# Optimization experiments

Measured on AMD Instinct MI355X. Metric: run time of the kernel, lower is better.

## Reference

```python
import jax, jax.numpy as jnp
import numpy as np

B, L, D, HD = 4, 4096, 2048, 128

def setup_inputs() -> dict:
    key = jax.random.key(0)
    ks = jax.random.split(key, 9)
    s = 0.02  # keep logits in a sane range
    return {
        "x": jax.random.normal(ks[0], (B, L, D), jnp.float32),
        "Wq": jax.random.normal(ks[1], (D, HD), jnp.float32) * s,
        "bq": jax.random.normal(ks[2], (HD,), jnp.float32) * s,
        "Wk": jax.random.normal(ks[3], (D, HD), jnp.float32) * s,
        "bk": jax.random.normal(ks[4], (HD,), jnp.float32) * s,
        "Wv": jax.random.normal(ks[5], (D, HD), jnp.float32) * s,
        "bv": jax.random.normal(ks[6], (HD,), jnp.float32) * s,
        "Wo": jax.random.normal(ks[7], (HD, D), jnp.float32) * s,
        "bo": jax.random.normal(ks[8], (D,), jnp.float32) * s,
    }

def reference(x, Wq, bq, Wk, bk, Wv, bv, Wo, bo):
    # x: (B, L, D)
    q = x @ Wq + bq                      # (B, L, HD)
    k = x @ Wk + bk
    v = x @ Wv + bv
    hd = q.shape[-1]
    scores = jnp.einsum('bqd,bkd->bqk', q, k) / jnp.sqrt(jnp.float32(hd))
    Lq = x.shape[1]
    causal = jnp.tril(jnp.ones((Lq, Lq), dtype=bool))  # (L, L)
    scores = jnp.where(causal, scores, -jnp.inf)
    weights = jax.nn.softmax(scores, axis=-1)          # (B, L, L)
    out = jnp.einsum('bqk,bkd->bqd', weights, v)       # (B, L, HD)
    return out @ Wo + bo                               # (B, L, D)
```

## Files before the change

kernel.cpp:

```cpp
#include <hip/hip_runtime.h>

#define B_  4
#define L_  4096
#define D_  2048
#define HD_ 128
#define M_  (B_*L_)

typedef __attribute__((ext_vector_type(8))) short short8;
typedef __attribute__((ext_vector_type(4))) float f32x4;
typedef __attribute__((ext_vector_type(16))) float f32x16;
typedef __attribute__((ext_vector_type(4))) unsigned short u16x4;
typedef __attribute__((ext_vector_type(4))) unsigned int u32x4;
typedef unsigned short u16;

__device__ __forceinline__ u16 f2bf(float f){
  union { float f; unsigned u; } v; v.f = f;
  unsigned r = v.u + 0x7FFFu + ((v.u >> 16) & 1u);
  return (u16)(r >> 16);
}

__device__ __forceinline__ unsigned cvtpk_bf16(float a, float b){
  unsigned r;
  asm volatile("v_cvt_pk_bf16_f32 %0, %1, %2" : "=v"(r) : "v"(a), "v"(b));
  return r;
}

__global__ __launch_bounds__(256) void prepw_kernel(
    const float* __restrict__ Wq, const float* __restrict__ Wk,
    const float* __restrict__ Wv, const float* __restrict__ Wo,
    u16* __restrict__ Wf_qkv, u16* __restrict__ Wf_o)
{
  __shared__ float T[64][68];
  const int tid = threadIdx.x;
  int tb = blockIdx.x;
  int mat = tb >> 6, tt = tb & 63;
  const float* src; int Cw, rt, ct;
  if (mat < 3) {
    src = (mat==0) ? Wq : (mat==1) ? Wk : Wv;
    Cw = HD_; rt = tt >> 1; ct = tt & 1;
  } else {
    src = Wo;
    Cw = D_; rt = tt >> 5; ct = tt & 31;
  }
  int r0 = rt*64, c0 = ct*64;
  #pragma unroll
  for (int i=0;i<4;i++){
    int fid = i*256 + tid;
    int row = fid >> 4, c4 = (fid & 15) * 4;
    float4 v = *reinterpret_cast<const float4*>(src + (size_t)(r0+row)*Cw + c0 + c4);
    *reinterpret_cast<float4*>(&T[row][c4]) = v;
  }
  __syncthreads();
  #pragma unroll
  for (int i=0;i<2;i++){
    int sid = i*256 + tid;
    int crow = sid >> 3, k8 = (sid & 7) * 8;
    short8 o;
    #pragma unroll
    for (int j=0;j<8;j++) o[j] = (short)f2bf(T[k8+j][crow]);
    int K = r0 + k8;
    if (mat < 3) {
      int C = mat*128 + c0 + crow;
      size_t off = ((size_t)(K>>4)*12 + (C>>5))*512
                 + ((((K>>3)&1))*32 + (C&31))*8;
      *reinterpret_cast<short8*>(Wf_qkv + off) = o;
    } else {
      int C = c0 + crow;
      size_t off = ((size_t)(K>>5)*128 + (C>>4))*512
                 + ((((K>>3)&3))*16 + (C&15))*8;
      *reinterpret_cast<short8*>(Wf_o + off) = o;
    }
  }
}

__global__ __launch_bounds__(256) void prepx_kernel(
    const float* __restrict__ x, u16* __restrict__ xbf)
{
  int cid  = blockIdx.x*4 + (threadIdx.x >> 6);
  int lane = threadIdx.x & 63;
  int l31 = lane & 31, hi = lane >> 5;
  int rs = cid >> 7, t = cid & 127;
  const float* src = x + (size_t)(rs*32 + l31)*D_ + t*16 + hi*8;
  float4 f0 = *reinterpret_cast<const float4*>(src);
  float4 f1 = *reinterpret_cast<const float4*>(src + 4);
  union { u32x4 u; short8 s8; } o;
  o.u[0] = cvtpk_bf16(f0.x, f0.y);
  o.u[1] = cvtpk_bf16(f0.z, f0.w);
  o.u[2] = cvtpk_bf16(f1.x, f1.y);
  o.u[3] = cvtpk_bf16(f1.z, f1.w);
  *reinterpret_cast<short8*>(xbf + (size_t)cid*512 + lane*8) = o.s8;
}

__global__ __launch_bounds__(256, 2) void qkv_kernel(
    const u16* __restrict__ xbf, const u16* __restrict__ Wf,
    const float* __restrict__ bq, const float* __restrict__ bk,
    const float* __restrict__ bv,
    u16* __restrict__ Q, u16* __restrict__ Kf, u16* __restrict__ Vf)
{
  const int rb = blockIdx.x;
  const int tid = threadIdx.x;
  const int lane = tid & 63, wc = tid >> 6;
  const int l31 = lane & 31, hi = lane >> 5;

  const u16* aP0 = xbf + ((size_t)(rb*2    )*128)*512 + lane*8;
  const u16* aP1 = xbf + ((size_t)(rb*2 + 1)*128)*512 + lane*8;
  const u16* bP  = Wf  + (size_t)(wc*3)*512 + lane*8;

  f32x16 acc[2][3];
  #pragma unroll
  for (int m=0;m<2;m++)
    #pragma unroll
    for (int nb=0;nb<3;nb++)
      #pragma unroll
      for (int i=0;i<16;i++) acc[m][nb][i] = 0.f;

  short8 a0 = *reinterpret_cast<const short8*>(aP0);
  short8 a1 = *reinterpret_cast<const short8*>(aP1);
  short8 b0 = *reinterpret_cast<const short8*>(bP);
  short8 b1 = *reinterpret_cast<const short8*>(bP + 512);
  short8 b2 = *reinterpret_cast<const short8*>(bP + 1024);

  for (int t = 0; t < 127; ++t) {
    short8 na0 = *reinterpret_cast<const short8*>(aP0 + (size_t)(t+1)*512);
    short8 na1 = *reinterpret_cast<const short8*>(aP1 + (size_t)(t+1)*512);
    const u16* nb_ = bP + (size_t)(t+1)*12*512;
    short8 nb0 = *reinterpret_cast<const short8*>(nb_);
    short8 nb1 = *reinterpret_cast<const short8*>(nb_ + 512);
    short8 nb2 = *reinterpret_cast<const short8*>(nb_ + 1024);
    __builtin_amdgcn_s_setprio(1);
    acc[0][0] = __builtin_amdgcn_mfma_f32_32x32x16_bf16(a0, b0, acc[0][0], 0, 0, 0);
    acc[0][1] = __builtin_amdgcn_mfma_f32_32x32x16_bf16(a0, b1, acc[0][1], 0, 0, 0);
    acc[0][2] = __builtin_amdgcn_mfma_f32_32x32x16_bf16(a0, b2, acc[0][2], 0, 0, 0);
    acc[1][0] = __builtin_amdgcn_mfma_f32_32x32x16_bf16(a1, b0, acc[1][0], 0, 0, 0);
    acc[1][1] = __builtin_amdgcn_mfma_f32_32x32x16_bf16(a1, b1, acc[1][1], 0, 0, 0);
    acc[1][2] = __builtin_amdgcn_mfma_f32_32x32x16_bf16(a1, b2, acc[1][2], 0, 0, 0);
    __builtin_amdgcn_s_setprio(0);
    a0 = na0; a1 = na1; b0 = nb0; b1 = nb1; b2 = nb2;
  }
  __builtin_amdgcn_s_setprio(1);
  acc[0][0] = __builtin_amdgcn_mfma_f32_32x32x16_bf16(a0, b0, acc[0][0], 0, 0, 0);
  acc[0][1] = __builtin_amdgcn_mfma_f32_32x32x16_bf16(a0, b1, acc[0][1], 0, 0, 0);
  acc[0][2] = __builtin_amdgcn_mfma_f32_32x32x16_bf16(a0, b2, acc[0][2], 0, 0, 0);
  acc[1][0] = __builtin_amdgcn_mfma_f32_32x32x16_bf16(a1, b0, acc[1][0], 0, 0, 0);
  acc[1][1] = __builtin_amdgcn_mfma_f32_32x32x16_bf16(a1, b1, acc[1][1], 0, 0, 0);
  acc[1][2] = __builtin_amdgcn_mfma_f32_32x32x16_bf16(a1, b2, acc[1][2], 0, 0, 0);
  __builtin_amdgcn_s_setprio(0);

  const float qscale = 0.08838834764831845f;
  const int bb = rb >> 6, kt = rb & 63;
  const size_t kvBase = ((size_t)bb*64 + kt)*16;
  #pragma unroll
  for (int nb=0; nb<3; nb++){
    const int colbase = wc*96 + nb*32;
    const int j = colbase >> 7;
    const int col = colbase + l31;
    const int c = col & 127;
    const float bi = (j==0) ? bq[c] : (j==1) ? bk[c] : bv[c];
    #pragma unroll
    for (int m=0;m<2;m++){
      if (j == 0) {
        #pragma unroll
        for (int r=0;r<16;r++){
          int row = rb*64 + m*32 + 4*hi + (r&3) + 8*(r>>2);
          Q[(size_t)row*HD_ + c] = f2bf((acc[m][nb][r] + bi) * qscale);
        }
      } else if (j == 1) {
        int ksd = c >> 4, hid = (c >> 3) & 1, jd = c & 7;
        #pragma unroll
        for (int r=0;r<16;r++){
          int l31k = 8*(r>>2) + 4*hi + (r&3);
          Kf[(kvBase + m*8 + ksd)*512 + (hid*32 + l31k)*8 + jd]
              = f2bf(acc[m][nb][r] + bi);
        }
      } else {
        int nbv = c >> 5;
        #pragma unroll
        for (int g=0; g<4; g++){
          int ksv = m*2 + (g>>1), hiv = g&1, j0 = 4*hi;
          u16x4 v4;
          #pragma unroll
          for (int q=0;q<4;q++) v4[q] = f2bf(acc[m][nb][4*g+q] + bi);
          *reinterpret_cast<u16x4*>(
              Vf + (kvBase + ksv*4 + nbv)*512 + (hiv*32 + l31)*8 + j0) = v4;
        }
      }
    }
  }
}

__global__ __launch_bounds__(256, 2) void attn_kernel(
    const u16* __restrict__ Qg, const u16* __restrict__ Kfg,
    const u16* __restrict__ Vfg, u16* __restrict__ AOf)
{
  const int blk = blockIdx.x;
  const int xcd = blk & 7;
  const int sub = blk >> 3;
  const int b   = xcd >> 1;
  const int strip = 127 - (2*sub + (xcd & 1));
  const int q0  = strip * 32;
  const int KT  = (strip >> 1) + 1;

  const int tid = threadIdx.x, lane = tid & 63, w = tid >> 6;
  const int l31 = lane & 31;
  const int hi  = lane >> 5;

  const u16* Qb  = Qg  + (size_t)b * L_ * HD_;
  const u16* Kfb = Kfg + (size_t)b * 64 * 8192 + lane*8;
  const u16* Vfb = Vfg + (size_t)b * 64 * 8192 + lane*8;

  __shared__ __attribute__((aligned(16))) float Ol[4][32][132];
  __shared__ float Ml[4][32], Ll[4][32];

  short8 qf[8];
  #pragma unroll
  for (int ks=0; ks<8; ks++)
    qf[ks] = *reinterpret_cast<const short8*>(
        &Qb[(size_t)(q0 + l31)*HD_ + ks*16 + hi*8]);

  f32x16 O[4];
  #pragma unroll
  for (int nb=0; nb<4; nb++)
    #pragma unroll
    for (int i=0;i<16;i++) O[nb][i] = 0.f;
  float m_ = -__builtin_inff();
  float l_ = 0.f;

  for (int kt = w; kt < KT; kt += 4) {
    const u16* Kt = Kfb + (size_t)kt*8192;
    f32x16 s[2];
    #pragma unroll
    for (int n=0;n<2;n++)
      #pragma unroll
      for (int i=0;i<16;i++) s[n][i] = 0.f;
    __builtin_amdgcn_s_setprio(1);
    #pragma unroll
    for (int ks=0;ks<8;ks++)
      #pragma unroll
      for (int n=0;n<2;n++){
        short8 ka = *reinterpret_cast<const short8*>(Kt + (n*8 + ks)*512);
        s[n] = __builtin_amdgcn_mfma_f32_32x32x16_bf16(ka, qf[ks], s[n], 0, 0, 0);
      }
    __builtin_amdgcn_s_setprio(0);

    if (kt == KT-1) {
      #pragma unroll
      for (int n=0;n<2;n++)
        #pragma unroll
        for (int reg=0;reg<16;reg++){
          int key = kt*64 + n*32 + (reg&3) + 8*(reg>>2) + 4*hi;
          if (key > q0 + l31) s[n][reg] = -__builtin_inff();
        }
    }

    float pmax = s[0][0];
    #pragma unroll
    for (int n=0;n<2;n++)
      #pragma unroll
      for (int reg=0;reg<16;reg++) pmax = fmaxf(pmax, s[n][reg]);
    pmax = fmaxf(pmax, __shfl_xor(pmax, 32, 64));

    if (!__all(pmax <= m_ + 8.f)) {
      float mnew = fmaxf(m_, pmax);
      float alpha = __expf(m_ - mnew);
      m_ = mnew;
      l_ *= alpha;
      #pragma unroll
      for (int nb=0; nb<4; nb++)
        #pragma unroll
        for (int i=0;i<16;i++) O[nb][i] *= alpha;
    }

    float rsum = 0.f;
    #pragma unroll
    for (int n=0;n<2;n++)
      #pragma unroll
      for (int reg=0;reg<16;reg++){
        float p = __expf(s[n][reg] - m_);
        s[n][reg] = p;
        rsum += p;
      }
    rsum += __shfl_xor(rsum, 32, 64);
    l_ += rsum;

    unsigned c[2][8], ox[2][8];
    #pragma unroll
    for (int n=0;n<2;n++)
      #pragma unroll
      for (int i=0;i<8;i++)
        c[n][i] = cvtpk_bf16(s[n][2*i], s[n][2*i+1]);
    #pragma unroll
    for (int n=0;n<2;n++)
      #pragma unroll
      for (int i=0;i<8;i++)
        ox[n][i] = (unsigned)__shfl_xor((int)c[n][i], 32, 64);

    short8 pb[4];
    #pragma unroll
    for (int n=0;n<2;n++)
      #pragma unroll
      for (int sB=0;sB<2;sB++){
        union { u32x4 u; short8 s8; } t;
        t.u[0] = hi ? ox[n][4*sB+2] : c[n][4*sB+0];
        t.u[1] = hi ? ox[n][4*sB+3] : c[n][4*sB+1];
        t.u[2] = hi ? c[n][4*sB+2]  : ox[n][4*sB+0];
        t.u[3] = hi ? c[n][4*sB+3]  : ox[n][4*sB+1];
        pb[2*n+sB] = t.s8;
      }

    const u16* Vt2 = Vfb + (size_t)kt*8192;
    __builtin_amdgcn_s_setprio(1);
    #pragma unroll
    for (int ks=0; ks<4; ks++){
      #pragma unroll
      for (int nb=0; nb<4; nb++){
        short8 av = *reinterpret_cast<const short8*>(Vt2 + (ks*4 + nb)*512);
        O[nb] = __builtin_amdgcn_mfma_f32_32x32x16_bf16(av, pb[ks], O[nb], 0, 0, 0);
      }
    }
    __builtin_amdgcn_s_setprio(0);
  }

  if (hi == 0) { Ml[w][l31] = m_; Ll[w][l31] = l_; }
  #pragma unroll
  for (int nb=0; nb<4; nb++)
    #pragma unroll
    for (int g=0; g<4; g++){
      f32x4 v;
      v[0]=O[nb][4*g+0]; v[1]=O[nb][4*g+1]; v[2]=O[nb][4*g+2]; v[3]=O[nb][4*g+3];
      *reinterpret_cast<f32x4*>(&Ol[w][l31][nb*32 + g*8 + hi*4]) = v;
    }
  __syncthreads();

  {
    int q  = tid >> 3;
    int dc = (tid & 7) * 16;
    float mw[4], lw[4];
    float M = -__builtin_inff();
    #pragma unroll
    for (int w2=0; w2<4; w2++){ mw[w2]=Ml[w2][q]; lw[w2]=Ll[w2][q]; M = fmaxf(M, mw[w2]); }
    float den = 0.f, cw[4];
    #pragma unroll
    for (int w2=0; w2<4; w2++){ float e = __expf(mw[w2]-M); cw[w2]=e; den += lw[w2]*e; }
    float inv = 1.0f/den;
    float o[16];
    #pragma unroll
    for (int j=0;j<16;j++) o[j] = 0.f;
    #pragma unroll
    for (int w2=0; w2<4; w2++){
      #pragma unroll
      for (int g=0; g<4; g++){
        f32x4 p = *reinterpret_cast<const f32x4*>(&Ol[w2][q][dc + g*4]);
        #pragma unroll
        for (int j=0;j<4;j++) o[g*4+j] += cw[w2]*p[j];
      }
    }
    short8 st0, st1;
    #pragma unroll
    for (int j=0;j<8;j++){ st0[j] = (short)f2bf(o[j]*inv); st1[j] = (short)f2bf(o[8+j]*inv); }
    size_t rowg = (size_t)b*L_ + q0 + q;
    size_t rb2g = rowg >> 5;
    int qq = (int)(rowg & 31);
    int mA = qq >> 4, l15A = qq & 15;
    int ks0 = dc >> 5,      lh0 = (dc >> 3) & 3;
    int ks1 = (dc+8) >> 5,  lh1 = ((dc+8) >> 3) & 3;
    *reinterpret_cast<short8*>(AOf + ((rb2g*4 + ks0)*2 + mA)*512 + (lh0*16 + l15A)*8) = st0;
    *reinterpret_cast<short8*>(AOf + ((rb2g*4 + ks1)*2 + mA)*512 + (lh1*16 + l15A)*8) = st1;
  }
}

__global__ __launch_bounds__(256) void proj_kernel(
    const u16* __restrict__ AOf, const u16* __restrict__ Wf_o,
    const float* __restrict__ bo, float* __restrict__ out)
{
  const int nb  = blockIdx.x;
  const int rbk = blockIdx.y;
  const int tid = threadIdx.x, lane = tid & 63, w = tid >> 6;
  const int l15 = lane & 15, lhi = lane >> 4;

  const u16* faBase = AOf  + (size_t)rbk*8*512 + lane*8;
  const u16* fbBase = Wf_o + lane*8;

  f32x4 acc[2][4];
  f32x4 zero4 = {0.f,0.f,0.f,0.f};
  #pragma unroll
  for (int m=0;m<2;m++)
    #pragma unroll
    for (int n=0;n<4;n++) acc[m][n] = zero4;

  #pragma unroll
  for (int ks=0; ks<4; ks++){
    short8 fa[2], fb[4];
    #pragma unroll
    for (int m=0;m<2;m++)
      fa[m] = *reinterpret_cast<const short8*>(faBase + (ks*2 + m)*512);
    #pragma unroll
    for (int n=0;n<4;n++)
      fb[n] = *reinterpret_cast<const short8*>(
          fbBase + (size_t)(ks*128 + nb*16 + w*4 + n)*512);
    #pragma unroll
    for (int m=0;m<2;m++)
      #pragma unroll
      for (int n=0;n<4;n++)
        acc[m][n] = __builtin_amdgcn_mfma_f32_16x16x32_bf16(fa[m], fb[n], acc[m][n], 0, 0, 0);
  }

  #pragma unroll
  for (int n=0;n<4;n++){
    int col = nb*256 + w*64 + n*16 + l15;
    float bi = bo[col];
    #pragma unroll
    for (int m=0;m<2;m++){
      int row = rbk*32 + m*16 + (lhi<<2);
      #pragma unroll
      for (int r=0;r<4;r++)
        out[(size_t)(row+r)*D_ + col] = acc[m][n][r] + bi;
    }
  }
}

extern "C" void kernel_launch(void* const* d_in, const int* in_sizes, int n_in,
                              void* d_out, int out_size, void* d_ws, size_t ws_size,
                              hipStream_t stream) {
  const float* x  = (const float*)d_in[0];
  const float* Wq = (const float*)d_in[1];
  const float* bq = (const float*)d_in[2];
  const float* Wk = (const float*)d_in[3];
  const float* bk = (const float*)d_in[4];
  const float* Wv = (const float*)d_in[5];
  const float* bv = (const float*)d_in[6];
  const float* Wo = (const float*)d_in[7];
  const float* bo = (const float*)d_in[8];
  float* out = (float*)d_out;

  u16* ws      = (u16*)d_ws;
  u16* Wf_qkv  = ws;
  u16* Wf_o    = Wf_qkv + 3*HD_*D_;
  u16* Q       = Wf_o   + (size_t)D_*HD_;
  u16* Kf      = Q + (size_t)M_*HD_;
  u16* Vf      = Kf + (size_t)M_*HD_;
  u16* AOf     = Vf + (size_t)M_*HD_;
  u16* xbf     = AOf + (size_t)M_*HD_;

  prepw_kernel<<<256, 256, 0, stream>>>(Wq, Wk, Wv, Wo, Wf_qkv, Wf_o);
  prepx_kernel<<<16384, 256, 0, stream>>>(x, xbf);
  qkv_kernel<<<256, 256, 0, stream>>>(xbf, Wf_qkv, bq, bk, bv, Q, Kf, Vf);
  attn_kernel<<<512, 256, 0, stream>>>(Q, Kf, Vf, AOf);
  proj_kernel<<<dim3(8, 512), 256, 0, stream>>>(AOf, Wf_o, bo, out);
}
```

Baseline: 195.8 us.

## Halve QKV row tile per block and deepen register prefetch pipeline

The QKV projection kernel now handles 32 rows per block instead of 64, so it launches 512 blocks instead of 256 and fills more of the GPU's compute units. The K loop becomes a double-buffered register pipeline that loads 4 k-steps of A and B fragments ahead, replacing the single-step prefetch. This aims to improve occupancy and hide global load latency better. In exchange, each weight fragment is reused by only one row tile, which doubles W traffic per output, and more registers are held live.

```diff
diff --git a/kernel.cpp b/kernel.cpp
--- a/kernel.cpp
+++ b/kernel.cpp
@@ -102,52 +102,69 @@
   const int lane = tid & 63, wc = tid >> 6;
   const int l31 = lane & 31, hi = lane >> 5;
 
-  const u16* aP0 = xbf + ((size_t)(rb*2    )*128)*512 + lane*8;
-  const u16* aP1 = xbf + ((size_t)(rb*2 + 1)*128)*512 + lane*8;
-  const u16* bP  = Wf  + (size_t)(wc*3)*512 + lane*8;
-
-  f32x16 acc[2][3];
-  #pragma unroll
-  for (int m=0;m<2;m++)
-    #pragma unroll
-    for (int nb=0;nb<3;nb++)
-      #pragma unroll
-      for (int i=0;i<16;i++) acc[m][nb][i] = 0.f;
-
-  short8 a0 = *reinterpret_cast<const short8*>(aP0);
-  short8 a1 = *reinterpret_cast<const short8*>(aP1);
-  short8 b0 = *reinterpret_cast<const short8*>(bP);
-  short8 b1 = *reinterpret_cast<const short8*>(bP + 512);
-  short8 b2 = *reinterpret_cast<const short8*>(bP + 1024);
-
-  for (int t = 0; t < 127; ++t) {
-    short8 na0 = *reinterpret_cast<const short8*>(aP0 + (size_t)(t+1)*512);
-    short8 na1 = *reinterpret_cast<const short8*>(aP1 + (size_t)(t+1)*512);
-    const u16* nb_ = bP + (size_t)(t+1)*12*512;
-    short8 nb0 = *reinterpret_cast<const short8*>(nb_);
-    short8 nb1 = *reinterpret_cast<const short8*>(nb_ + 512);
-    short8 nb2 = *reinterpret_cast<const short8*>(nb_ + 1024);
+  const u16* aP = xbf + ((size_t)rb*128)*512 + lane*8;
+  const u16* bP = Wf  + (size_t)(wc*3)*512 + lane*8;
+
+  f32x16 acc[3];
+  #pragma unroll
+  for (int nb=0;nb<3;nb++)
+    #pragma unroll
+    for (int i=0;i<16;i++) acc[nb][i] = 0.f;
+
+  short8 gaA[4], gbA[4][3], gaB[4], gbB[4][3];
+
+  #pragma unroll
+  for (int s=0;s<4;s++){
+    gaA[s] = *reinterpret_cast<const short8*>(aP + (size_t)s*512);
+    #pragma unroll
+    for (int n=0;n<3;n++)
+      gbA[s][n] = *reinterpret_cast<const short8*>(bP + ((size_t)s*12 + n)*512);
+  }
+
+  #pragma unroll 1
+  for (int g = 0; g < 32; g += 2) {
+    if (g + 1 < 32) {
+      const u16* ap = aP + (size_t)(g+1)*4*512;
+      const u16* bp = bP + (size_t)(g+1)*48*512;
+      #pragma unroll
+      for (int s=0;s<4;s++){
+        gaB[s] = *reinterpret_cast<const short8*>(ap + (size_t)s*512);
+        #pragma unroll
+        for (int n=0;n<3;n++)
+          gbB[s][n] = *reinterpret_cast<const short8*>(bp + ((size_t)s*12 + n)*512);
+      }
+    }
     __builtin_amdgcn_s_setprio(1);
-    acc[0][0] = __builtin_amdgcn_mfma_f32_32x32x16_bf16(a0, b0, acc[0][0], 0, 0, 0);
-    acc[0][1] = __builtin_amdgcn_mfma_f32_32x32x16_bf16(a0, b1, acc[0][1], 0, 0, 0);
-    acc[0][2] = __builtin_amdgcn_mfma_f32_32x32x16_bf16(a0, b2, acc[0][2], 0, 0, 0);
-    acc[1][0] = __builtin_amdgcn_mfma_f32_32x32x16_bf16(a1, b0, acc[1][0], 0, 0, 0);
-    acc[1][1] = __builtin_amdgcn_mfma_f32_32x32x16_bf16(a1, b1, acc[1][1], 0, 0, 0);
-    acc[1][2] = __builtin_amdgcn_mfma_f32_32x32x16_bf16(a1, b2, acc[1][2], 0, 0, 0);
+    #pragma unroll
+    for (int s=0;s<4;s++)
+      #pragma unroll
+      for (int n=0;n<3;n++)
+        acc[n] = __builtin_amdgcn_mfma_f32_32x32x16_bf16(gaA[s], gbA[s][n], acc[n], 0, 0, 0);
     __builtin_amdgcn_s_setprio(0);
-    a0 = na0; a1 = na1; b0 = nb0; b1 = nb1; b2 = nb2;
-  }
-  __builtin_amdgcn_s_setprio(1);
-  acc[0][0] = __builtin_amdgcn_mfma_f32_32x32x16_bf16(a0, b0, acc[0][0], 0, 0, 0);
-  acc[0][1] = __builtin_amdgcn_mfma_f32_32x32x16_bf16(a0, b1, acc[0][1], 0, 0, 0);
-  acc[0][2] = __builtin_amdgcn_mfma_f32_32x32x16_bf16(a0, b2, acc[0][2], 0, 0, 0);
-  acc[1][0] = __builtin_amdgcn_mfma_f32_32x32x16_bf16(a1, b0, acc[1][0], 0, 0, 0);
-  acc[1][1] = __builtin_amdgcn_mfma_f32_32x32x16_bf16(a1, b1, acc[1][1], 0, 0, 0);
-  acc[1][2] = __builtin_amdgcn_mfma_f32_32x32x16_bf16(a1, b2, acc[1][2], 0, 0, 0);
-  __builtin_amdgcn_s_setprio(0);
+    if (g + 2 < 32) {
+      const u16* ap = aP + (size_t)(g+2)*4*512;
+      const u16* bp = bP + (size_t)(g+2)*48*512;
+      #pragma unroll
+      for (int s=0;s<4;s++){
+        gaA[s] = *reinterpret_cast<const short8*>(ap + (size_t)s*512);
+        #pragma unroll
+        for (int n=0;n<3;n++)
+          gbA[s][n] = *reinterpret_cast<const short8*>(bp + ((size_t)s*12 + n)*512);
+      }
+    }
+    __builtin_amdgcn_s_setprio(1);
+    #pragma unroll
+    for (int s=0;s<4;s++)
+      #pragma unroll
+      for (int n=0;n<3;n++)
+        acc[n] = __builtin_amdgcn_mfma_f32_32x32x16_bf16(gaB[s], gbB[s][n], acc[n], 0, 0, 0);
+    __builtin_amdgcn_s_setprio(0);
+  }
 
   const float qscale = 0.08838834764831845f;
-  const int bb = rb >> 6, kt = rb & 63;
+  const int bb = rb >> 7;
+  const int kt = (rb & 127) >> 1;
+  const int n2 = rb & 1;
   const size_t kvBase = ((size_t)bb*64 + kt)*16;
   #pragma unroll
   for (int nb=0; nb<3; nb++){
@@ -156,33 +173,30 @@
     const int col = colbase + l31;
     const int c = col & 127;
     const float bi = (j==0) ? bq[c] : (j==1) ? bk[c] : bv[c];
-    #pragma unroll
-    for (int m=0;m<2;m++){
-      if (j == 0) {
-        #pragma unroll
-        for (int r=0;r<16;r++){
-          int row = rb*64 + m*32 + 4*hi + (r&3) + 8*(r>>2);
-          Q[(size_t)row*HD_ + c] = f2bf((acc[m][nb][r] + bi) * qscale);
-        }
-      } else if (j == 1) {
-        int ksd = c >> 4, hid = (c >> 3) & 1, jd = c & 7;
-        #pragma unroll
-        for (int r=0;r<16;r++){
-          int l31k = 8*(r>>2) + 4*hi + (r&3);
-          Kf[(kvBase + m*8 + ksd)*512 + (hid*32 + l31k)*8 + jd]
-              = f2bf(acc[m][nb][r] + bi);
-        }
-      } else {
-        int nbv = c >> 5;
-        #pragma unroll
-        for (int g=0; g<4; g++){
-          int ksv = m*2 + (g>>1), hiv = g&1, j0 = 4*hi;
-          u16x4 v4;
-          #pragma unroll
-          for (int q=0;q<4;q++) v4[q] = f2bf(acc[m][nb][4*g+q] + bi);
-          *reinterpret_cast<u16x4*>(
-              Vf + (kvBase + ksv*4 + nbv)*512 + (hiv*32 + l31)*8 + j0) = v4;
-        }
+    if (j == 0) {
+      #pragma unroll
+      for (int r=0;r<16;r++){
+        int row = rb*32 + 4*hi + (r&3) + 8*(r>>2);
+        Q[(size_t)row*HD_ + c] = f2bf((acc[nb][r] + bi) * qscale);
+      }
+    } else if (j == 1) {
+      int ksd = c >> 4, hid = (c >> 3) & 1, jd = c & 7;
+      #pragma unroll
+      for (int r=0;r<16;r++){
+        int l31k = 8*(r>>2) + 4*hi + (r&3);
+        Kf[(kvBase + n2*8 + ksd)*512 + (hid*32 + l31k)*8 + jd]
+            = f2bf(acc[nb][r] + bi);
+      }
+    } else {
+      int nbv = c >> 5;
+      #pragma unroll
+      for (int g2=0; g2<4; g2++){
+        int ksv = n2*2 + (g2>>1), hiv = g2&1, j0 = 4*hi;
+        u16x4 v4;
+        #pragma unroll
+        for (int q=0;q<4;q++) v4[q] = f2bf(acc[nb][4*g2+q] + bi);
+        *reinterpret_cast<u16x4*>(
+            Vf + (kvBase + ksv*4 + nbv)*512 + (hiv*32 + l31)*8 + j0) = v4;
       }
     }
   }
@@ -443,7 +457,7 @@
 
   prepw_kernel<<<256, 256, 0, stream>>>(Wq, Wk, Wv, Wo, Wf_qkv, Wf_o);
   prepx_kernel<<<16384, 256, 0, stream>>>(x, xbf);
-  qkv_kernel<<<256, 256, 0, stream>>>(xbf, Wf_qkv, bq, bk, bv, Q, Kf, Vf);
+  qkv_kernel<<<512, 256, 0, stream>>>(xbf, Wf_qkv, bq, bk, bv, Q, Kf, Vf);
   attn_kernel<<<512, 256, 0, stream>>>(Q, Kf, Vf, AOf);
   proj_kernel<<<dim3(8, 512), 256, 0, stream>>>(AOf, Wf_o, bo, out);
 }
```

After: 191.2 us. 1.02x faster.
